# Performance work log

Hardware: AMD Instinct MI355X
Metric: run time of the kernel (lower is better)

The kernel has to match this reference:

```python
import jax, jax.numpy as jnp
import numpy as np

D_IN = 4096
D_OUT = 4096
RANK = 16
ALPHA = 32
SCALE = ALPHA / RANK


def setup_inputs() -> dict:
    key = jax.random.key(0)
    k_x, k_w, k_b, k_a = jax.random.split(key, 4)
    x = jax.random.normal(k_x, (4, 2048, D_IN), dtype=jnp.float32)
    weight = jax.random.normal(k_w, (D_OUT, D_IN), dtype=jnp.float32) * (1.0 / np.sqrt(D_IN))
    bias = jax.random.normal(k_b, (D_OUT,), dtype=jnp.float32)
    lora_A = jax.random.normal(k_a, (RANK, D_IN), dtype=jnp.float32) * 0.01
    lora_B = jnp.zeros((D_OUT, RANK), dtype=jnp.float32)
    return {"x": x, "weight": weight, "bias": bias, "lora_A": lora_A, "lora_B": lora_B}


def reference(x, weight, bias, lora_A, lora_B):
    # base linear: y = x @ W^T + b   -> [B, S, D_OUT]
    orig_out = jnp.einsum("bsd,od->bso", x, weight) + bias
    # low-rank path: (x @ A^T) @ B^T * (alpha/rank)
    lora_out = jnp.einsum("bsr,or->bso", jnp.einsum("bsd,rd->bsr", x, lora_A), lora_B)
    return orig_out + lora_out * SCALE
```

## Files before the change

### kernel.cpp

```cpp
#include <hip/hip_runtime.h>
#include <stdint.h>

#define DIN   4096
#define DOUT  4096
#define RANK  16
#define MTOT  8192
#define LSCALE 2.0f

typedef unsigned short u16;
typedef __bf16 bf16x8 __attribute__((ext_vector_type(8)));
typedef float  f32x4  __attribute__((ext_vector_type(4)));
typedef u16    u16x8  __attribute__((ext_vector_type(8)));

__device__ __forceinline__ u16 f2bf(float f) {
    uint32_t u = __builtin_bit_cast(uint32_t, f);
    u = (u + 0x7FFFu + ((u >> 16) & 1u)) >> 16;
    return (u16)u;
}

__device__ __forceinline__ u16x8 pack8(f32x4 a, f32x4 b) {
    u16x8 o;
    o[0] = f2bf(a[0]); o[1] = f2bf(a[1]); o[2] = f2bf(a[2]); o[3] = f2bf(a[3]);
    o[4] = f2bf(b[0]); o[5] = f2bf(b[1]); o[6] = f2bf(b[2]); o[7] = f2bf(b[3]);
    return o;
}

#define GLDS16(g, l) __builtin_amdgcn_global_load_lds( \
    (const __attribute__((address_space(1))) void*)(g), \
    (__attribute__((address_space(3))) void*)(l), 16, 0, 0)

__global__ __launch_bounds__(256) void k_convert_x(const float* __restrict__ x,
                                                   u16* __restrict__ xb) {
    long i = ((long)blockIdx.x * 256 + threadIdx.x) * 8;
    f32x4 a = *(const f32x4*)(x + i);
    f32x4 b = *(const f32x4*)(x + i + 4);
    *(u16x8*)(xb + i) = pack8(a, b);
}

__global__ __launch_bounds__(256) void k_build_weff(const float* __restrict__ W,
                                                    const float* __restrict__ A,
                                                    const float* __restrict__ B,
                                                    u16* __restrict__ wb) {
    long t = (long)blockIdx.x * 256 + threadIdx.x;
    long i = t * 8;
    int o = (int)(i >> 12);
    int d = (int)(i & (DIN - 1));
    float sB[RANK];
#pragma unroll
    for (int r = 0; r < RANK; ++r) sB[r] = B[o * RANK + r] * LSCALE;
    f32x4 w0 = *(const f32x4*)(W + i);
    f32x4 w1 = *(const f32x4*)(W + i + 4);
#pragma unroll
    for (int r = 0; r < RANK; ++r) {
        f32x4 a0 = *(const f32x4*)(A + (long)r * DIN + d);
        f32x4 a1 = *(const f32x4*)(A + (long)r * DIN + d + 4);
        w0 += a0 * sB[r];
        w1 += a1 * sB[r];
    }
    *(u16x8*)(wb + i) = pack8(w0, w1);
}

#define BM 256
#define BN 256
#define BK 64
#define NT (DIN / BK)

#define MFMA16(d, a, b) d = __builtin_amdgcn_mfma_f32_16x16x32_bf16(a, b, d, 0, 0, 0)
#define RAWBAR() __builtin_amdgcn_s_barrier()

__global__ __launch_bounds__(512, 2) void k_gemm_ws(const u16* __restrict__ xb,
                                                    const u16* __restrict__ wb,
                                                    const float* __restrict__ bias,
                                                    float* __restrict__ out) {
    constexpr int K = DIN, N = DOUT;
    constexpr int AT = BM * BK;
    constexpr int BT = BN * BK;
    __shared__ alignas(16) u16 lds[2 * (AT + BT)];

    const int nchunk = gridDim.x >> 3;
    const int bid = blockIdx.x;
    const int wg  = (bid & 7) * nchunk + (bid >> 3);
    const int bm  = (wg & 31) * BM;
    const int bn  = (wg >> 5) * BN;

    const int tid  = threadIdx.x;
    const int lane = tid & 63;
    const int wid  = tid >> 6;
    const int wr   = wid >> 2;
    const int wc   = wid & 3;
    const int lrow = lane & 15;
    const int kgrp = lane >> 4;

    const int srow = tid >> 3;
    const int sgl  = (tid & 7) ^ (srow & 7);
    const u16* aSrc = xb + (long)(bm + srow) * K + sgl * 8;
    const u16* bSrc = wb + (long)(bn + srow) * K + sgl * 8;
    u16* const dA0 = lds            + tid * 8;
    u16* const dA1 = lds + AT       + tid * 8;
    u16* const dB0 = lds + 2*AT     + tid * 8;
    u16* const dB1 = lds + 2*AT+BT  + tid * 8;

    const int gg  = kgrp ^ (lrow & 7);
    const int go0 = gg * 8;
    const int go1 = (gg ^ 4) * 8;
    const u16* const rA0 = lds            + (wr*128 + lrow) * BK;
    const u16* const rA1 = lds + AT       + (wr*128 + lrow) * BK;
    const u16* const rB0 = lds + 2*AT     + (wc*64  + lrow) * BK;
    const u16* const rB1 = lds + 2*AT+BT  + (wc*64  + lrow) * BK;

    f32x4 acc[8][4];
#pragma unroll
    for (int m = 0; m < 8; ++m)
#pragma unroll
        for (int n = 0; n < 4; ++n) acc[m][n] = (f32x4){0.f, 0.f, 0.f, 0.f};

    {
        const u16* s = aSrc;
        GLDS16(s, dA0); GLDS16(s + 64*K, dA0 + 4096);
        GLDS16(s + 128*K, dA0 + 8192); GLDS16(s + 192*K, dA0 + 12288);
        const u16* p = bSrc;
        GLDS16(p, dB0); GLDS16(p + 64*K, dB0 + 4096);
        GLDS16(p + 128*K, dB0 + 8192); GLDS16(p + 192*K, dB0 + 12288);
    }
    asm volatile("s_waitcnt vmcnt(0)" ::: "memory");
    __syncthreads();

    for (int t = 0; t < NT; ++t) {
        const int cur = t & 1;
        const u16* cA = cur ? rA1 : rA0;
        const u16* cB = cur ? rB1 : rB0;
        u16* nA = cur ? dA0 : dA1;
        u16* nB = cur ? dB0 : dB1;
        const int tn = (t + 1) & (NT - 1);

        bf16x8 afL[4][2], afH[4][2], bfA[2][2], bfB[2][2];

#pragma unroll
        for (int m = 0; m < 4; ++m) {
            afL[m][0] = *(const bf16x8*)(cA + m*1024 + go0);
            afL[m][1] = *(const bf16x8*)(cA + m*1024 + go1);
        }
#pragma unroll
        for (int n = 0; n < 2; ++n) {
            bfA[n][0] = *(const bf16x8*)(cB + n*1024 + go0);
            bfA[n][1] = *(const bf16x8*)(cB + n*1024 + go1);
        }
        {
            const u16* s = aSrc + tn * BK;
            GLDS16(s, nA); GLDS16(s + 64*K, nA + 4096);
            GLDS16(s + 128*K, nA + 8192); GLDS16(s + 192*K, nA + 12288);
        }
        RAWBAR();
        __builtin_amdgcn_s_setprio(1);
#pragma unroll
        for (int m = 0; m < 4; ++m)
#pragma unroll
            for (int n = 0; n < 2; ++n) {
                MFMA16(acc[m][n], afL[m][0], bfA[n][0]);
                MFMA16(acc[m][n], afL[m][1], bfA[n][1]);
            }
        __builtin_amdgcn_s_setprio(0);
        RAWBAR();

#pragma unroll
        for (int n = 0; n < 2; ++n) {
            bfB[n][0] = *(const bf16x8*)(cB + (n+2)*1024 + go0);
            bfB[n][1] = *(const bf16x8*)(cB + (n+2)*1024 + go1);
        }
        {
            const u16* s = bSrc + tn * BK;
            GLDS16(s, nB); GLDS16(s + 64*K, nB + 4096);
            GLDS16(s + 128*K, nB + 8192); GLDS16(s + 192*K, nB + 12288);
        }
        RAWBAR();
        __builtin_amdgcn_s_setprio(1);
#pragma unroll
        for (int m = 0; m < 4; ++m)
#pragma unroll
            for (int n = 0; n < 2; ++n) {
                MFMA16(acc[m][n+2], afL[m][0], bfB[n][0]);
                MFMA16(acc[m][n+2], afL[m][1], bfB[n][1]);
            }
        __builtin_amdgcn_s_setprio(0);
        RAWBAR();

#pragma unroll
        for (int m = 0; m < 4; ++m) {
            afH[m][0] = *(const bf16x8*)(cA + (m+4)*1024 + go0);
            afH[m][1] = *(const bf16x8*)(cA + (m+4)*1024 + go1);
        }
        RAWBAR();
        __builtin_amdgcn_s_setprio(1);
#pragma unroll
        for (int m = 0; m < 4; ++m)
#pragma unroll
            for (int n = 0; n < 2; ++n) {
                MFMA16(acc[m+4][n+2], afH[m][0], bfB[n][0]);
                MFMA16(acc[m+4][n+2], afH[m][1], bfB[n][1]);
            }
        __builtin_amdgcn_s_setprio(0);
        RAWBAR();

        asm volatile("s_waitcnt vmcnt(0)" ::: "memory");
        RAWBAR();
        __builtin_amdgcn_s_setprio(1);
#pragma unroll
        for (int m = 0; m < 4; ++m)
#pragma unroll
            for (int n = 0; n < 2; ++n) {
                MFMA16(acc[m+4][n], afH[m][0], bfA[n][0]);
                MFMA16(acc[m+4][n], afH[m][1], bfA[n][1]);
            }
        __builtin_amdgcn_s_setprio(0);
        RAWBAR();
    }

    const int orow = bm + wr*128 + kgrp*4;
    const int ocol = bn + wc*64 + lrow;
#pragma unroll
    for (int n = 0; n < 4; ++n) {
        const float bj = bias[ocol + n*16];
#pragma unroll
        for (int m = 0; m < 8; ++m) {
#pragma unroll
            for (int r = 0; r < 4; ++r)
                out[(long)(orow + m*16 + r) * N + (ocol + n*16)] = acc[m][n][r] + bj;
        }
    }
}

__global__ __launch_bounds__(64) void k_lora_T(const float* __restrict__ x,
                                               const float* __restrict__ A,
                                               float* __restrict__ T) {
    const int m = blockIdx.x;
    const int lane = threadIdx.x;
    const float* xr = x + (long)m * DIN;
    float acc[RANK];
#pragma unroll
    for (int r = 0; r < RANK; ++r) acc[r] = 0.f;
    for (int k = lane * 4; k < DIN; k += 64 * 4) {
        f32x4 xv = *(const f32x4*)(xr + k);
#pragma unroll
        for (int r = 0; r < RANK; ++r) {
            f32x4 av = *(const f32x4*)(A + (long)r * DIN + k);
            acc[r] += xv[0] * av[0] + xv[1] * av[1] + xv[2] * av[2] + xv[3] * av[3];
        }
    }
#pragma unroll
    for (int r = 0; r < RANK; ++r)
        for (int off = 32; off > 0; off >>= 1) acc[r] += __shfl_down(acc[r], off);
    if (lane == 0) {
#pragma unroll
        for (int r = 0; r < RANK; ++r) T[(long)m * RANK + r] = acc[r] * LSCALE;
    }
}

__global__ __launch_bounds__(256) void k_gemm_nows(const float* __restrict__ x,
                                                   const float* __restrict__ W,
                                                   const float* __restrict__ bias,
                                                   const float* __restrict__ T,
                                                   const float* __restrict__ lB,
                                                   float* __restrict__ out) {
    constexpr int FBM = 128, FBN = 128, FBK = 32, K = DIN, N = DOUT;
    __shared__ __align__(16) u16 As[FBM * FBK];
    __shared__ __align__(16) u16 Bs[FBN * FBK];

    const int tid = threadIdx.x;
    const int bm = blockIdx.y * FBM;
    const int bn = blockIdx.x * FBN;
    const int lane = tid & 63;
    const int wid  = tid >> 6;
    const int wr = wid >> 1, wc = wid & 1;
    const int lrow = lane & 15;
    const int kgrp = lane >> 4;

    const int c0 = tid, c1 = tid + 256;
    const float* aS0 = x + (long)(bm + (c0 >> 2)) * K + (c0 & 3) * 8;
    const float* aS1 = x + (long)(bm + (c1 >> 2)) * K + (c1 & 3) * 8;
    const float* bS0 = W + (long)(bn + (c0 >> 2)) * K + (c0 & 3) * 8;
    const float* bS1 = W + (long)(bn + (c1 >> 2)) * K + (c1 & 3) * 8;
    u16* aD0 = As + c0 * 8;  u16* aD1 = As + c1 * 8;
    u16* bD0 = Bs + c0 * 8;  u16* bD1 = Bs + c1 * 8;

    const u16* aR = As + (wr * 64 + lrow) * FBK + kgrp * 8;
    const u16* bR = Bs + (wc * 64 + lrow) * FBK + kgrp * 8;

    f32x4 acc[4][4];
#pragma unroll
    for (int i = 0; i < 4; ++i)
#pragma unroll
        for (int j = 0; j < 4; ++j) acc[i][j] = (f32x4){0.f, 0.f, 0.f, 0.f};

    for (int k0 = 0; k0 < K; k0 += FBK) {
        f32x4 a00 = *(const f32x4*)aS0, a01 = *(const f32x4*)(aS0 + 4);
        f32x4 a10 = *(const f32x4*)aS1, a11 = *(const f32x4*)(aS1 + 4);
        f32x4 b00 = *(const f32x4*)bS0, b01 = *(const f32x4*)(bS0 + 4);
        f32x4 b10 = *(const f32x4*)bS1, b11 = *(const f32x4*)(bS1 + 4);
        aS0 += FBK; aS1 += FBK; bS0 += FBK; bS1 += FBK;
        if (k0) __syncthreads();
        *(u16x8*)aD0 = pack8(a00, a01);
        *(u16x8*)aD1 = pack8(a10, a11);
        *(u16x8*)bD0 = pack8(b00, b01);
        *(u16x8*)bD1 = pack8(b10, b11);
        __syncthreads();

        bf16x8 af[4], bf[4];
#pragma unroll
        for (int i = 0; i < 4; ++i) af[i] = *(const bf16x8*)(aR + i * 16 * FBK);
#pragma unroll
        for (int j = 0; j < 4; ++j) bf[j] = *(const bf16x8*)(bR + j * 16 * FBK);
#pragma unroll
        for (int i = 0; i < 4; ++i)
#pragma unroll
            for (int j = 0; j < 4; ++j)
                acc[i][j] = __builtin_amdgcn_mfma_f32_16x16x32_bf16(af[i], bf[j], acc[i][j], 0, 0, 0);
    }

#pragma unroll
    for (int j = 0; j < 4; ++j) {
        const int col = bn + wc * 64 + j * 16 + lrow;
        const float bj = bias[col];
        float bl[RANK];
#pragma unroll
        for (int q = 0; q < RANK; ++q) bl[q] = lB[(long)col * RANK + q];
#pragma unroll
        for (int i = 0; i < 4; ++i) {
            const int row0 = bm + wr * 64 + i * 16 + kgrp * 4;
#pragma unroll
            for (int r = 0; r < 4; ++r) {
                const int row = row0 + r;
                const float* Trow = T + (long)row * RANK;
                float s = bj;
#pragma unroll
                for (int q = 0; q < RANK; ++q) s += Trow[q] * bl[q];
                out[(long)row * N + col] = acc[i][j][r] + s;
            }
        }
    }
}

extern "C" void kernel_launch(void* const* d_in, const int* in_sizes, int n_in,
                              void* d_out, int out_size, void* d_ws, size_t ws_size,
                              hipStream_t stream) {
    const float* x    = (const float*)d_in[0];
    const float* W    = (const float*)d_in[1];
    const float* bias = (const float*)d_in[2];
    const float* lA   = (const float*)d_in[3];
    const float* lB   = (const float*)d_in[4];
    float* out = (float*)d_out;

    const size_t xb_bytes = (size_t)MTOT * DIN * sizeof(u16);
    const size_t wb_bytes = (size_t)DOUT * DIN * sizeof(u16);

    if (ws_size >= xb_bytes + wb_bytes) {
        u16* xb = (u16*)d_ws;
        u16* wb = (u16*)((char*)d_ws + xb_bytes);
        k_convert_x <<<(int)((long)MTOT * DIN / 8 / 256), 256, 0, stream>>>(x, xb);
        k_build_weff<<<(int)((long)DOUT * DIN / 8 / 256), 256, 0, stream>>>(W, lA, lB, wb);
        k_gemm_ws   <<<(MTOT / BM) * (DOUT / BN), 512, 0, stream>>>(xb, wb, bias, out);
    } else {
        float* T = (float*)d_ws;
        k_lora_T   <<<MTOT, 64, 0, stream>>>(x, lA, T);
        k_gemm_nows<<<dim3(DOUT / 128, MTOT / 128), 256, 0, stream>>>(x, W, bias, T, lB, out);
    }
}
```

Measured before the change: 343.1 us.

## Split tile loads into quarter-chunks with staggered vmcnt waits and remapped warp tiles

Global-to-LDS staging of the next K tile is broken into 64-row chunks issued across the four MFMA phases, each followed by a partial vmcnt(4) wait, replacing the single full drain before the last phase. Warp-to-tile mapping changes so each warp owns two separated 64x32 quadrants (rows wr*64 and +128, cols wc*32 and +128) instead of a contiguous 128x64 block, so each phase only reads the chunks already staged. This spreads memory traffic over the iteration to overlap with compute. The cost is tighter dependence ordering, where a wrong wait count would silently read stale LDS, plus a less contiguous output store pattern.

```diff
diff --git a/kernel.cpp b/kernel.cpp
--- a/kernel.cpp
+++ b/kernel.cpp
@@ -67,15 +67,14 @@
 
 #define MFMA16(d, a, b) d = __builtin_amdgcn_mfma_f32_16x16x32_bf16(a, b, d, 0, 0, 0)
 #define RAWBAR() __builtin_amdgcn_s_barrier()
+#define VMCNT4() asm volatile("s_waitcnt vmcnt(4)" ::: "memory")
 
 __global__ __launch_bounds__(512, 2) void k_gemm_ws(const u16* __restrict__ xb,
                                                     const u16* __restrict__ wb,
                                                     const float* __restrict__ bias,
                                                     float* __restrict__ out) {
     constexpr int K = DIN, N = DOUT;
-    constexpr int AT = BM * BK;
-    constexpr int BT = BN * BK;
-    __shared__ alignas(16) u16 lds[2 * (AT + BT)];
+    __shared__ alignas(16) u16 lds[65536];
 
     const int nchunk = gridDim.x >> 3;
     const int bid = blockIdx.x;
@@ -93,20 +92,20 @@
 
     const int srow = tid >> 3;
     const int sgl  = (tid & 7) ^ (srow & 7);
-    const u16* aSrc = xb + (long)(bm + srow) * K + sgl * 8;
-    const u16* bSrc = wb + (long)(bn + srow) * K + sgl * 8;
-    u16* const dA0 = lds            + tid * 8;
-    u16* const dA1 = lds + AT       + tid * 8;
-    u16* const dB0 = lds + 2*AT     + tid * 8;
-    u16* const dB1 = lds + 2*AT+BT  + tid * 8;
-
-    const int gg  = kgrp ^ (lrow & 7);
-    const int go0 = gg * 8;
-    const int go1 = (gg ^ 4) * 8;
-    const u16* const rA0 = lds            + (wr*128 + lrow) * BK;
-    const u16* const rA1 = lds + AT       + (wr*128 + lrow) * BK;
-    const u16* const rB0 = lds + 2*AT     + (wc*64  + lrow) * BK;
-    const u16* const rB1 = lds + 2*AT+BT  + (wc*64  + lrow) * BK;
+    const u16* const aSrcB = xb + (long)(bm + srow) * K + sgl * 8;
+    const u16* const bSrcB = wb + (long)(bn + srow) * K + sgl * 8;
+
+#define STAGE_A(c, buf, kt) GLDS16(aSrcB + (long)(64*(c))*K + (kt)*BK, \
+                                   lds + (buf)*16384 + (c)*4096 + tid*8)
+#define STAGE_B(c, buf, kt) GLDS16(bSrcB + (long)(64*(c))*K + (kt)*BK, \
+                                   lds + 32768 + (buf)*16384 + (c)*4096 + tid*8)
+
+    const int go0 = (kgrp ^ (lrow & 7)) * 8;
+    const int go1 = go0 ^ 32;
+    const int arL = (wr*64 + lrow) * 64;
+    const int arH = arL + 128*64;
+    const int brL = (wc*32 + lrow) * 64;
+    const int brH = brL + 128*64;
 
     f32x4 acc[8][4];
 #pragma unroll
@@ -114,42 +113,32 @@
 #pragma unroll
         for (int n = 0; n < 4; ++n) acc[m][n] = (f32x4){0.f, 0.f, 0.f, 0.f};
 
-    {
-        const u16* s = aSrc;
-        GLDS16(s, dA0); GLDS16(s + 64*K, dA0 + 4096);
-        GLDS16(s + 128*K, dA0 + 8192); GLDS16(s + 192*K, dA0 + 12288);
-        const u16* p = bSrc;
-        GLDS16(p, dB0); GLDS16(p + 64*K, dB0 + 4096);
-        GLDS16(p + 128*K, dB0 + 8192); GLDS16(p + 192*K, dB0 + 12288);
-    }
+    STAGE_A(0, 0, 0); STAGE_A(1, 0, 0);
+    STAGE_B(0, 0, 0); STAGE_B(1, 0, 0);
+    STAGE_B(2, 0, 0); STAGE_B(3, 0, 0);
+    STAGE_A(2, 0, 0); STAGE_A(3, 0, 0);
     asm volatile("s_waitcnt vmcnt(0)" ::: "memory");
     __syncthreads();
 
     for (int t = 0; t < NT; ++t) {
-        const int cur = t & 1;
-        const u16* cA = cur ? rA1 : rA0;
-        const u16* cB = cur ? rB1 : rB0;
-        u16* nA = cur ? dA0 : dA1;
-        u16* nB = cur ? dB0 : dB1;
+        const int cur = t & 1, nxt = cur ^ 1;
         const int tn = (t + 1) & (NT - 1);
+        const u16* const pA = lds + cur*16384;
+        const u16* const pB = lds + 32768 + cur*16384;
 
         bf16x8 afL[4][2], afH[4][2], bfA[2][2], bfB[2][2];
 
 #pragma unroll
         for (int m = 0; m < 4; ++m) {
-            afL[m][0] = *(const bf16x8*)(cA + m*1024 + go0);
-            afL[m][1] = *(const bf16x8*)(cA + m*1024 + go1);
+            afL[m][0] = *(const bf16x8*)(pA + arL + m*1024 + go0);
+            afL[m][1] = *(const bf16x8*)(pA + arL + m*1024 + go1);
         }
 #pragma unroll
         for (int n = 0; n < 2; ++n) {
-            bfA[n][0] = *(const bf16x8*)(cB + n*1024 + go0);
-            bfA[n][1] = *(const bf16x8*)(cB + n*1024 + go1);
-        }
-        {
-            const u16* s = aSrc + tn * BK;
-            GLDS16(s, nA); GLDS16(s + 64*K, nA + 4096);
-            GLDS16(s + 128*K, nA + 8192); GLDS16(s + 192*K, nA + 12288);
-        }
+            bfA[n][0] = *(const bf16x8*)(pB + brL + n*1024 + go0);
+            bfA[n][1] = *(const bf16x8*)(pB + brL + n*1024 + go1);
+        }
+        STAGE_A(0, nxt, tn); STAGE_A(1, nxt, tn);
         RAWBAR();
         __builtin_amdgcn_s_setprio(1);
 #pragma unroll
@@ -160,18 +149,15 @@
                 MFMA16(acc[m][n], afL[m][1], bfA[n][1]);
             }
         __builtin_amdgcn_s_setprio(0);
+        VMCNT4();
         RAWBAR();
 
 #pragma unroll
         for (int n = 0; n < 2; ++n) {
-            bfB[n][0] = *(const bf16x8*)(cB + (n+2)*1024 + go0);
-            bfB[n][1] = *(const bf16x8*)(cB + (n+2)*1024 + go1);
-        }
-        {
-            const u16* s = bSrc + tn * BK;
-            GLDS16(s, nB); GLDS16(s + 64*K, nB + 4096);
-            GLDS16(s + 128*K, nB + 8192); GLDS16(s + 192*K, nB + 12288);
-        }
+            bfB[n][0] = *(const bf16x8*)(pB + brH + n*1024 + go0);
+            bfB[n][1] = *(const bf16x8*)(pB + brH + n*1024 + go1);
+        }
+        STAGE_B(0, nxt, tn); STAGE_B(1, nxt, tn);
         RAWBAR();
         __builtin_amdgcn_s_setprio(1);
 #pragma unroll
@@ -182,13 +168,15 @@
                 MFMA16(acc[m][n+2], afL[m][1], bfB[n][1]);
             }
         __builtin_amdgcn_s_setprio(0);
+        VMCNT4();
         RAWBAR();
 
 #pragma unroll
         for (int m = 0; m < 4; ++m) {
-            afH[m][0] = *(const bf16x8*)(cA + (m+4)*1024 + go0);
-            afH[m][1] = *(const bf16x8*)(cA + (m+4)*1024 + go1);
-        }
+            afH[m][0] = *(const bf16x8*)(pA + arH + m*1024 + go0);
+            afH[m][1] = *(const bf16x8*)(pA + arH + m*1024 + go1);
+        }
+        STAGE_B(2, nxt, tn); STAGE_B(3, nxt, tn);
         RAWBAR();
         __builtin_amdgcn_s_setprio(1);
 #pragma unroll
@@ -201,7 +189,7 @@
         __builtin_amdgcn_s_setprio(0);
         RAWBAR();
 
-        asm volatile("s_waitcnt vmcnt(0)" ::: "memory");
+        STAGE_A(2, nxt, tn); STAGE_A(3, nxt, tn);
         RAWBAR();
         __builtin_amdgcn_s_setprio(1);
 #pragma unroll
@@ -212,19 +200,23 @@
                 MFMA16(acc[m+4][n], afH[m][1], bfA[n][1]);
             }
         __builtin_amdgcn_s_setprio(0);
-        RAWBAR();
-    }
-
-    const int orow = bm + wr*128 + kgrp*4;
-    const int ocol = bn + wc*64 + lrow;
+        VMCNT4();
+        RAWBAR();
+    }
+    asm volatile("s_waitcnt vmcnt(0)" ::: "memory");
+
+    const int orow = bm + wr*64 + kgrp*4;
+    const int ocol = bn + wc*32 + lrow;
 #pragma unroll
     for (int n = 0; n < 4; ++n) {
-        const float bj = bias[ocol + n*16];
+        const int col = ocol + (n & 1)*16 + (n >> 1)*128;
+        const float bj = bias[col];
 #pragma unroll
         for (int m = 0; m < 8; ++m) {
+            const int row = orow + (m & 3)*16 + (m >> 2)*128;
 #pragma unroll
             for (int r = 0; r < 4; ++r)
-                out[(long)(orow + m*16 + r) * N + (ocol + n*16)] = acc[m][n][r] + bj;
+                out[(long)(row + r) * N + col] = acc[m][n][r] + bj;
         }
     }
 }
```

New measurement: 331.1 us. 1.04x faster.
